# Optimization experiments

Hardware: AMD Instinct MI355X
Metric: run time of the kernel (lower is better)

## Reference

```python
import jax, jax.numpy as jnp
import numpy as np

NEG = -1e9


def _lstm_step(x, h, c, W_ih, W_hh, b_ih, b_hh):
    # torch LSTM gate order: i, f, g, o
    gates = x @ W_ih.T + b_ih + h @ W_hh.T + b_hh
    i, f, g, o = jnp.split(gates, 4, axis=-1)
    c_new = jax.nn.sigmoid(f) * c + jax.nn.sigmoid(i) * jnp.tanh(g)
    h_new = jax.nn.sigmoid(o) * jnp.tanh(c_new)
    return h_new, c_new


def _forward(encoder_states, emb, W_ih, W_hh, b_ih, b_hh, W_att,
             pad_mask, pointer_mask, token_ids, target_sequence,
             sos_token, eos_token, output_len):
    B, N, D = encoder_states.shape
    V = emb.shape[0]
    dt = encoder_states.dtype
    padf = pad_mask.astype(dt)
    enc = encoder_states * padf[..., None]          # zero padded node states
    # _init_lstm_state: mean of encoder states over valid nodes (pad-only mask)
    h0 = enc.sum(axis=1) / padf.sum(axis=1, keepdims=True)  # [B, D]
    # attention mask after pointer restriction: only valid leaf pointer nodes
    attn_mask = jnp.where(pointer_mask, jnp.asarray(0.0, dt), jnp.asarray(NEG, dt))
    n_ptr = pointer_mask.sum(axis=1).astype(dt)     # [B]
    thr = 1.0 / n_ptr                               # _threshold_cf = 1.0
    b_idx = jnp.arange(B)

    # teacher forcing: step 1 uses SOS, step s>1 uses target_sequence[s-1]
    sos_row = jnp.full((1, B), sos_token, dtype=target_sequence.dtype)
    inputs = jnp.concatenate([sos_row, target_sequence[1:output_len - 1]], axis=0)  # [T-1, B]

    def step(carry, inp):
        h, c = carry
        x = emb[inp]                                     # [B, E]
        h, c = _lstm_step(x, h, c, W_ih, W_hh, b_ih, b_hh)
        # Luong attention -> probabilities over tree nodes
        scores = jnp.einsum('bnd,bd->bn', enc, h @ W_att.T) + attn_mask
        probs = jax.nn.softmax(scores, axis=1)           # [B, N]
        # threshold: probabilities below 1/n_ptr are zeroed; only pointer nodes kept
        probs = jnp.where(pointer_mask & (probs >= thr[:, None]), probs, jnp.asarray(0.0, dt))
        # scatter(reduce='sum') node probabilities into vocab-sized output
        out = jnp.zeros((B, V), dt).at[b_idx[:, None], token_ids].add(probs)
        out = out.at[:, eos_token].set(1.0 - probs.sum(axis=1))
        return (h, c), out

    (_, _), outs = jax.lax.scan(step, (h0, h0), inputs)   # [T-1, B, V]
    out0 = jnp.zeros((B, V), dt).at[:, sos_token].set(1.0)
    return jnp.concatenate([out0[None], outs], axis=0)    # [T, B, V]


def setup_inputs() -> dict:
    key = jax.random.key(0)
    ks = jax.random.split(key, 10)
    B, N, D, E, V, T = 32, 2048, 512, 512, 32000, 32
    encoder_states = jax.random.normal(ks[0], (B, N, D), dtype=jnp.float32)
    lengths = jax.random.randint(ks[1], (B,), N // 2, N + 1)
    pad_mask = jnp.arange(N)[None, :] < lengths[:, None]            # [B, N] ragged trees
    leaf = jax.random.bernoulli(ks[2], 0.5, (B, N))
    pointer_mask = pad_mask & leaf                                  # valid leaf pointer nodes
    token_ids = jax.random.randint(ks[3], (B, N), 0, V, dtype=jnp.int32)
    target_sequence = jax.random.randint(ks[4], (T, B), 3, V, dtype=jnp.int32)
    s = 0.02
    emb = jax.random.normal(ks[5], (V, E), dtype=jnp.float32) * s
    W_ih = jax.random.normal(ks[6], (4 * D, E), dtype=jnp.float32) * s
    W_hh = jax.random.normal(ks[7], (4 * D, D), dtype=jnp.float32) * s
    b_ih = jnp.zeros((4 * D,), dtype=jnp.float32)
    b_hh = jnp.zeros((4 * D,), dtype=jnp.float32)
    W_att = jax.random.normal(ks[8], (D, D), dtype=jnp.float32) * s
    return {
        'encoder_states': encoder_states, 'emb': emb,
        'W_ih': W_ih, 'W_hh': W_hh, 'b_ih': b_ih, 'b_hh': b_hh, 'W_att': W_att,
        'pad_mask': pad_mask, 'pointer_mask': pointer_mask,
        'token_ids': token_ids, 'target_sequence': target_sequence,
        'sos_token': 1, 'eos_token': 2, 'output_len': T,
    }


def reference(encoder_states, emb, W_ih, W_hh, b_ih, b_hh, W_att,
              pad_mask, pointer_mask, token_ids, target_sequence,
              sos_token, eos_token, output_len):
    return _forward(encoder_states, emb, W_ih, W_hh, b_ih, b_hh, W_att,
                    pad_mask, pointer_mask, token_ids, target_sequence,
                    sos_token, eos_token, output_len)
```

## Files before the change

### kernel.cpp

```cpp
#include <hip/hip_runtime.h>
#include <math.h>

#define BB 32
#define NN 2048
#define DD 512
#define VV 32000
#define NSTEP 31

__device__ inline float sigm(float x){ return 1.0f/(1.0f+expf(-x)); }
__device__ inline float dot4(float4 a, float4 b){
  return a.x*b.x + a.y*b.y + a.z*b.z + a.w*b.w;
}

__device__ inline float red8(float a0,float a1,float a2,float a3,
                             float a4,float a5,float a6,float a7,int lane){
  float m01 = ((lane&1)? a1:a0) + __shfl_xor(((lane&1)? a0:a1),1,64);
  float m23 = ((lane&1)? a3:a2) + __shfl_xor(((lane&1)? a2:a3),1,64);
  float m45 = ((lane&1)? a5:a4) + __shfl_xor(((lane&1)? a4:a5),1,64);
  float m67 = ((lane&1)? a7:a6) + __shfl_xor(((lane&1)? a6:a7),1,64);
  float m03 = ((lane&2)? m23:m01) + __shfl_xor(((lane&2)? m01:m23),2,64);
  float m47 = ((lane&2)? m67:m45) + __shfl_xor(((lane&2)? m45:m67),2,64);
  float m   = ((lane&4)? m47:m03) + __shfl_xor(((lane&4)? m03:m47),4,64);
  m += __shfl_xor(m,8,64); m += __shfl_xor(m,16,64); m += __shfl_xor(m,32,64);
  return m;
}

__global__ __launch_bounds__(256) void k_cnt(
    const int* __restrict__ pad, const int* __restrict__ pmask,
    const int* __restrict__ sosp,
    float* __restrict__ cntp, float* __restrict__ thr, float* __restrict__ out,
    unsigned int* __restrict__ flags) {
  __shared__ int r1[256], r2[256];
  int b = blockIdx.x, tid = threadIdx.x;
  if (b == 0 && tid <= 256)
    __hip_atomic_store(&flags[tid], 0u, __ATOMIC_RELAXED,
                       __HIP_MEMORY_SCOPE_AGENT);
  float4* orow4 = (float4*)(out + (size_t)b*VV);
  float4 z = {0.f,0.f,0.f,0.f};
  for (int i = tid; i < VV/4; i += 256) orow4[i] = z;
  int cp = 0, cq = 0;
  for (int n = tid; n < NN; n += 256) { cp += pad[b*NN+n]; cq += pmask[b*NN+n]; }
  r1[tid] = cp; r2[tid] = cq; __syncthreads();
  for (int st = 128; st; st >>= 1) {
    if (tid < st) { r1[tid] += r1[tid+st]; r2[tid] += r2[tid+st]; }
    __syncthreads();
  }
  if (tid == 0) {
    cntp[b] = (float)r1[0];
    thr[b]  = 1.0f/(float)r2[0];
    out[(size_t)b*VV + sosp[0]] = 1.0f;
  }
}

__global__ __launch_bounds__(128) void k_meanpart(
    const float* __restrict__ enc, const int* __restrict__ pad,
    float* __restrict__ hpart) {
  int b = blockIdx.x, ch = blockIdx.y, kq = threadIdx.x;
  int n0 = ch*32;
  float4 acc = {0.f,0.f,0.f,0.f};
#pragma unroll 8
  for (int r = 0; r < 32; r++) {
    int n = n0 + r;
    float msk = (float)pad[b*NN + n];
    float4 v = *(const float4*)(enc + ((size_t)(b*NN + n))*DD + kq*4);
    acc.x += msk*v.x; acc.y += msk*v.y; acc.z += msk*v.z; acc.w += msk*v.w;
  }
  *(float4*)(hpart + ((size_t)(b*64 + ch))*DD + kq*4) = acc;
}

__global__ __launch_bounds__(128) void k_meanfin(
    const float* __restrict__ hpart, const float* __restrict__ cntp,
    float* __restrict__ h0, float* __restrict__ c) {
  int b = blockIdx.x, kq = threadIdx.x;
  float4 acc = {0.f,0.f,0.f,0.f};
  for (int ch = 0; ch < 64; ch++) {
    float4 v = *(const float4*)(hpart + ((size_t)(b*64 + ch))*DD + kq*4);
    acc.x += v.x; acc.y += v.y; acc.z += v.z; acc.w += v.w;
  }
  float ic = 1.0f/cntp[b];
  acc.x *= ic; acc.y *= ic; acc.z *= ic; acc.w *= ic;
  *(float4*)(h0 + b*DD + kq*4) = acc;
  *(float4*)(c  + b*DD + kq*4) = acc;
}

__global__ __launch_bounds__(256) void k_g0(
    const float* __restrict__ emb, const float* __restrict__ Wih,
    const float* __restrict__ bih, const float* __restrict__ bhh,
    const int* __restrict__ target, const int* __restrict__ sosp,
    float* __restrict__ G0) {
  int nt = blockIdx.x, mg = blockIdx.y;
  int w = threadIdx.x>>6, lane = threadIdx.x&63;
  int m0 = mg*32 + w*8;
  float4 x0[8], x1[8];
#pragma unroll
  for (int j = 0; j < 8; j++) {
    int m = m0 + j, s = m >> 5, bb = m & 31;
    int tok = (s == 0) ? sosp[0] : target[s*BB + bb];
    const float* xp = emb + (size_t)tok*DD + lane*4;
    x0[j] = *(const float4*)xp;
    x1[j] = *(const float4*)(xp + 256);
  }
  int r0 = nt*32;
#pragma unroll 2
  for (int i = 0; i < 32; i++) {
    int r = r0 + i;
    const float* wp = Wih + (size_t)r*DD + lane*4;
    float4 w0 = *(const float4*)wp, w1 = *(const float4*)(wp + 256);
    float a0 = dot4(w0,x0[0]) + dot4(w1,x1[0]);
    float a1 = dot4(w0,x0[1]) + dot4(w1,x1[1]);
    float a2 = dot4(w0,x0[2]) + dot4(w1,x1[2]);
    float a3 = dot4(w0,x0[3]) + dot4(w1,x1[3]);
    float a4 = dot4(w0,x0[4]) + dot4(w1,x1[4]);
    float a5 = dot4(w0,x0[5]) + dot4(w1,x1[5]);
    float a6 = dot4(w0,x0[6]) + dot4(w1,x1[6]);
    float a7 = dot4(w0,x0[7]) + dot4(w1,x1[7]);
    float v = red8(a0,a1,a2,a3,a4,a5,a6,a7,lane) + bih[r] + bhh[r];
    if (lane < 8) G0[(size_t)(m0 + lane)*2048 + r] = v;
  }
}

__global__ __launch_bounds__(512, 2) void k_hloop(
    const float* __restrict__ h0, const float* __restrict__ Whh,
    const float* __restrict__ G0, float* __restrict__ H,
    unsigned int* __restrict__ flags) {
  __shared__ float pad[20736];
  float* g = pad;
  int bi = blockIdx.x, d0 = bi*2;
  int tid = threadIdx.x;
  int w = tid>>6, lane = tid&63;
  float4 W0[8], W1[8];
#pragma unroll
  for (int j = 0; j < 8; j++) {
    int r = (j>>1)*DD + d0 + (j&1);
    const float* wp = Whh + (size_t)r*DD + lane*4;
    W0[j] = *(const float4*)wp; W1[j] = *(const float4*)(wp + 256);
  }
  int pb = tid>>1, pdd = tid&1;
  float creg = 0.f;
  if (tid < 64) creg = h0[pb*DD + d0 + pdd];

  for (int s = 0; s < NSTEP; s++) {
#pragma unroll
    for (int j = 0; j < 8; j++) {
      asm volatile("" : "+v"(W0[j].x), "+v"(W0[j].y),
                        "+v"(W0[j].z), "+v"(W0[j].w),
                        "+v"(W1[j].x), "+v"(W1[j].y),
                        "+v"(W1[j].z), "+v"(W1[j].w));
    }
    const float* hin = (s == 0) ? h0 : (H + (size_t)(s-1)*BB*DD);
    float Gi = 0.f, Gf = 0.f, Gg = 0.f, Go = 0.f;
    if (tid < 64) {
      const float* G = G0 + ((size_t)s*BB + pb)*2048 + d0 + pdd;
      Gi = G[0]; Gf = G[512]; Gg = G[1024]; Go = G[1536];
    }
#pragma unroll
    for (int bb = 0; bb < 4; bb++) {
      int b = w*4 + bb;
      const float* hp = hin + b*DD + lane*4;
      float4 h0v = *(const float4*)hp, h1v = *(const float4*)(hp + 256);
      float a0 = dot4(h0v,W0[0]) + dot4(h1v,W1[0]);
      float a1 = dot4(h0v,W0[1]) + dot4(h1v,W1[1]);
      float a2 = dot4(h0v,W0[2]) + dot4(h1v,W1[2]);
      float a3 = dot4(h0v,W0[3]) + dot4(h1v,W1[3]);
      float a4 = dot4(h0v,W0[4]) + dot4(h1v,W1[4]);
      float a5 = dot4(h0v,W0[5]) + dot4(h1v,W1[5]);
      float a6 = dot4(h0v,W0[6]) + dot4(h1v,W1[6]);
      float a7 = dot4(h0v,W0[7]) + dot4(h1v,W1[7]);
      float v = red8(a0,a1,a2,a3,a4,a5,a6,a7,lane);
      if (lane < 8) g[b*8 + lane] = v;
    }
    __syncthreads();
    if (tid < 64) {
      float gi = g[pb*8 + 0 + pdd] + Gi;
      float gf = g[pb*8 + 2 + pdd] + Gf;
      float gg = g[pb*8 + 4 + pdd] + Gg;
      float go = g[pb*8 + 6 + pdd] + Go;
      creg = sigm(gf)*creg + sigm(gi)*tanhf(gg);
      float hn = sigm(go)*tanhf(creg);
      __hip_atomic_store(H + (size_t)s*BB*DD + pb*DD + d0 + pdd, hn,
                         __ATOMIC_RELAXED, __HIP_MEMORY_SCOPE_AGENT);
    }
    if (s == NSTEP-1) break;
    __syncthreads();
    unsigned tgt = (unsigned)(s+1);
    if (tid == 0)
      __hip_atomic_store(&flags[bi], tgt,
                         __ATOMIC_RELAXED, __HIP_MEMORY_SCOPE_AGENT);
    if (bi == 0 && tid < 64) {
      const unsigned int* fp = flags + tid*4;
      for (;;) {
        unsigned f0 = __hip_atomic_load(fp+0, __ATOMIC_RELAXED,
                                        __HIP_MEMORY_SCOPE_AGENT);
        unsigned f1 = __hip_atomic_load(fp+1, __ATOMIC_RELAXED,
                                        __HIP_MEMORY_SCOPE_AGENT);
        unsigned f2 = __hip_atomic_load(fp+2, __ATOMIC_RELAXED,
                                        __HIP_MEMORY_SCOPE_AGENT);
        unsigned f3 = __hip_atomic_load(fp+3, __ATOMIC_RELAXED,
                                        __HIP_MEMORY_SCOPE_AGENT);
        if (f0 >= tgt && f1 >= tgt && f2 >= tgt && f3 >= tgt) break;
        __builtin_amdgcn_s_sleep(1);
      }
      if (tid == 0)
        __hip_atomic_store(&flags[256], tgt,
                           __ATOMIC_RELAXED, __HIP_MEMORY_SCOPE_AGENT);
    }
    if (tid == 0) {
      while (__hip_atomic_load(&flags[256], __ATOMIC_RELAXED,
                               __HIP_MEMORY_SCOPE_AGENT) < tgt)
        __builtin_amdgcn_s_sleep(1);
    }
    __syncthreads();
    if (tid == 0) {
      unsigned acq = __hip_atomic_load(&flags[256], __ATOMIC_ACQUIRE,
                                       __HIP_MEMORY_SCOPE_AGENT);
      asm volatile("" :: "v"(acq));
    }
    __syncthreads();
  }
}

__global__ __launch_bounds__(256) void k_qallw(
    const float* __restrict__ H, const float* __restrict__ Watt,
    float* __restrict__ Q) {
  int nt = blockIdx.x, mg = blockIdx.y;
  int w = threadIdx.x>>6, lane = threadIdx.x&63;
  int m0 = mg*32 + w*8;
  float4 x0[8], x1[8];
#pragma unroll
  for (int j = 0; j < 8; j++) {
    const float* xp = H + (size_t)(m0 + j)*DD + lane*4;
    x0[j] = *(const float4*)xp; x1[j] = *(const float4*)(xp + 256);
  }
  int r0 = nt*16;
#pragma unroll 2
  for (int i = 0; i < 16; i++) {
    int r = r0 + i;
    const float* wp = Watt + (size_t)r*DD + lane*4;
    float4 w0 = *(const float4*)wp, w1 = *(const float4*)(wp + 256);
    float a0 = dot4(w0,x0[0]) + dot4(w1,x1[0]);
    float a1 = dot4(w0,x0[1]) + dot4(w1,x1[1]);
    float a2 = dot4(w0,x0[2]) + dot4(w1,x1[2]);
    float a3 = dot4(w0,x0[3]) + dot4(w1,x1[3]);
    float a4 = dot4(w0,x0[4]) + dot4(w1,x1[4]);
    float a5 = dot4(w0,x0[5]) + dot4(w1,x1[5]);
    float a6 = dot4(w0,x0[6]) + dot4(w1,x1[6]);
    float a7 = dot4(w0,x0[7]) + dot4(w1,x1[7]);
    float v = red8(a0,a1,a2,a3,a4,a5,a6,a7,lane);
    if (lane < 8) Q[(size_t)(m0 + lane)*DD + r] = v;
  }
}

__global__ __launch_bounds__(256) void k_scores3(
    const float* __restrict__ enc, const float* __restrict__ Q,
    float* __restrict__ S) {
  int nt = blockIdx.x, b = blockIdx.y;
  int w = threadIdx.x>>6, lane = threadIdx.x&63;
  int s0 = w*8;
  float4 q0[8], q1[8];
#pragma unroll
  for (int j = 0; j < 8; j++) {
    const float* qp = Q + (size_t)((s0 + j)*BB + b)*DD + lane*4;
    q0[j] = *(const float4*)qp; q1[j] = *(const float4*)(qp + 256);
  }
  int n0 = nt*32;
  int sl = s0 + (lane & 7);
#pragma unroll 2
  for (int i = 0; i < 32; i++) {
    int n = n0 + i;
    const float* ep = enc + ((size_t)(b*NN + n))*DD + lane*4;
    float4 e0 = *(const float4*)ep, e1 = *(const float4*)(ep + 256);
    float a0 = dot4(e0,q0[0]) + dot4(e1,q1[0]);
    float a1 = dot4(e0,q0[1]) + dot4(e1,q1[1]);
    float a2 = dot4(e0,q0[2]) + dot4(e1,q1[2]);
    float a3 = dot4(e0,q0[3]) + dot4(e1,q1[3]);
    float a4 = dot4(e0,q0[4]) + dot4(e1,q1[4]);
    float a5 = dot4(e0,q0[5]) + dot4(e1,q1[5]);
    float a6 = dot4(e0,q0[6]) + dot4(e1,q1[6]);
    float a7 = dot4(e0,q0[7]) + dot4(e1,q1[7]);
    float v = red8(a0,a1,a2,a3,a4,a5,a6,a7,lane);
    if (lane < 8 && sl < NSTEP) S[((size_t)sl*BB + b)*NN + n] = v;
  }
}

__global__ __launch_bounds__(256) void k_scatter2(
    const float* __restrict__ S, const int* __restrict__ pmask,
    const int* __restrict__ tok, const float* __restrict__ thr,
    const int* __restrict__ eosp, float* __restrict__ out) {
  __shared__ float red[256];
  __shared__ float ex[NN];
  int s = blockIdx.x, b = blockIdx.y, tid = threadIdx.x;
  float* orow = out + ((size_t)(s+1)*BB + b)*VV;
  float4 z = {0.f,0.f,0.f,0.f};
  float4* orow4 = (float4*)orow;
  for (int i = tid; i < VV/4; i += 256) orow4[i] = z;
  const float* sr = S + ((size_t)s*BB + b)*NN;
  const int* pm = pmask + b*NN;
  float m = -3.4e38f;
  for (int n = tid; n < NN; n += 256) if (pm[n]) m = fmaxf(m, sr[n]);
  red[tid] = m; __syncthreads();
  for (int st = 128; st; st >>= 1) {
    if (tid < st) red[tid] = fmaxf(red[tid], red[tid+st]);
    __syncthreads();
  }
  float smax = red[0]; __syncthreads();
  float sum = 0.f;
  for (int n = tid; n < NN; n += 256) {
    float e = pm[n] ? expf(sr[n] - smax) : 0.f;
    ex[n] = e; sum += e;
  }
  red[tid] = sum; __syncthreads();
  for (int st = 128; st; st >>= 1) {
    if (tid < st) red[tid] += red[tid+st];
    __syncthreads();
  }
  float inv = 1.0f/red[0];
  float th = thr[b];
  float keep = 0.f;
  for (int n = tid; n < NN; n += 256) {
    float p = ex[n]*inv;
    if (p >= th) { atomicAdd(orow + tok[b*NN + n], p); keep += p; }
  }
  __syncthreads();
  red[tid] = keep; __syncthreads();
  for (int st = 128; st; st >>= 1) {
    if (tid < st) red[tid] += red[tid+st];
    __syncthreads();
  }
  if (tid == 0) orow[eosp[0]] = 1.0f - red[0];
}

extern "C" void kernel_launch(void* const* d_in, const int* in_sizes, int n_in,
                              void* d_out, int out_size, void* d_ws, size_t ws_size,
                              hipStream_t stream) {
  const float* enc   = (const float*)d_in[0];
  const float* emb   = (const float*)d_in[1];
  const float* Wih   = (const float*)d_in[2];
  const float* Whh   = (const float*)d_in[3];
  const float* bih   = (const float*)d_in[4];
  const float* bhh   = (const float*)d_in[5];
  const float* Watt  = (const float*)d_in[6];
  const int*   pad   = (const int*)d_in[7];
  const int*   pmask = (const int*)d_in[8];
  const int*   tok   = (const int*)d_in[9];
  const int*   target= (const int*)d_in[10];
  const int*   sosp  = (const int*)d_in[11];
  const int*   eosp  = (const int*)d_in[12];
  float* out = (float*)d_out;

  float* w    = (float*)d_ws;
  float* c    = w;
  float* h0   = c    + BB*DD;
  float* H    = h0   + BB*DD;
  float* Q    = H    + NSTEP*BB*DD;
  float* S    = Q    + 32*BB*DD;
  float* G0   = S    + (size_t)NSTEP*BB*NN;
  float* cntp = G0   + (size_t)992*2048;
  float* thr  = cntp + 32;
  unsigned int* flags = (unsigned int*)(thr + 32);
  float* hpart = G0;

  k_cnt<<<32, 256, 0, stream>>>(pad, pmask, sosp, cntp, thr, out, flags);
  k_meanpart<<<dim3(32,64), 128, 0, stream>>>(enc, pad, hpart);
  k_meanfin<<<32, 128, 0, stream>>>(hpart, cntp, h0, c);

  k_g0<<<dim3(64,31), 256, 0, stream>>>(emb, Wih, bih, bhh, target, sosp, G0);

  k_hloop<<<256, 512, 0, stream>>>(h0, Whh, G0, H, flags);

  k_qallw<<<dim3(32,31), 256, 0, stream>>>(H, Watt, Q);
  k_scores3<<<dim3(64,32), 256, 0, stream>>>(enc, Q, S);
  k_scatter2<<<dim3(NSTEP,32), 256, 0, stream>>>(S, pmask, tok, thr, eosp, out);
}
```

Before: 667.0 us.

## Fuse input-gate projection into persistent LSTM loop and overlap with grid barrier

Removes the separate k_g0 kernel that precomputed x@W_ih for all steps. Each persistent k_hloop block now keeps its W_ih slice in registers and computes the next step's input gates while waiting at the grid barrier, double-buffering them in shared memory. It also drops one barrier/acquire stage in the step sync and fixes the flag-reset range. The cost is doubled register pressure, which may cause spills, and relaxed-only ordering on the H reads after the barrier.

```diff
diff --git a/kernel.cpp b/kernel.cpp
--- a/kernel.cpp
+++ b/kernel.cpp
@@ -32,9 +32,14 @@
     unsigned int* __restrict__ flags) {
   __shared__ int r1[256], r2[256];
   int b = blockIdx.x, tid = threadIdx.x;
-  if (b == 0 && tid <= 256)
-    __hip_atomic_store(&flags[tid], 0u, __ATOMIC_RELAXED,
-                       __HIP_MEMORY_SCOPE_AGENT);
+  if (b == 0) {
+    if (tid < 256)
+      __hip_atomic_store(&flags[tid], 0u, __ATOMIC_RELAXED,
+                         __HIP_MEMORY_SCOPE_AGENT);
+    if (tid == 0)
+      __hip_atomic_store(&flags[256], 0u, __ATOMIC_RELAXED,
+                         __HIP_MEMORY_SCOPE_AGENT);
+  }
   float4* orow4 = (float4*)(out + (size_t)b*VV);
   float4 z = {0.f,0.f,0.f,0.f};
   for (int i = tid; i < VV/4; i += 256) orow4[i] = z;
@@ -83,61 +88,54 @@
   *(float4*)(c  + b*DD + kq*4) = acc;
 }
 
-__global__ __launch_bounds__(256) void k_g0(
-    const float* __restrict__ emb, const float* __restrict__ Wih,
-    const float* __restrict__ bih, const float* __restrict__ bhh,
-    const int* __restrict__ target, const int* __restrict__ sosp,
-    float* __restrict__ G0) {
-  int nt = blockIdx.x, mg = blockIdx.y;
-  int w = threadIdx.x>>6, lane = threadIdx.x&63;
-  int m0 = mg*32 + w*8;
-  float4 x0[8], x1[8];
-#pragma unroll
-  for (int j = 0; j < 8; j++) {
-    int m = m0 + j, s = m >> 5, bb = m & 31;
-    int tok = (s == 0) ? sosp[0] : target[s*BB + bb];
-    const float* xp = emb + (size_t)tok*DD + lane*4;
-    x0[j] = *(const float4*)xp;
-    x1[j] = *(const float4*)(xp + 256);
-  }
-  int r0 = nt*32;
-#pragma unroll 2
-  for (int i = 0; i < 32; i++) {
-    int r = r0 + i;
-    const float* wp = Wih + (size_t)r*DD + lane*4;
-    float4 w0 = *(const float4*)wp, w1 = *(const float4*)(wp + 256);
-    float a0 = dot4(w0,x0[0]) + dot4(w1,x1[0]);
-    float a1 = dot4(w0,x0[1]) + dot4(w1,x1[1]);
-    float a2 = dot4(w0,x0[2]) + dot4(w1,x1[2]);
-    float a3 = dot4(w0,x0[3]) + dot4(w1,x1[3]);
-    float a4 = dot4(w0,x0[4]) + dot4(w1,x1[4]);
-    float a5 = dot4(w0,x0[5]) + dot4(w1,x1[5]);
-    float a6 = dot4(w0,x0[6]) + dot4(w1,x1[6]);
-    float a7 = dot4(w0,x0[7]) + dot4(w1,x1[7]);
-    float v = red8(a0,a1,a2,a3,a4,a5,a6,a7,lane) + bih[r] + bhh[r];
-    if (lane < 8) G0[(size_t)(m0 + lane)*2048 + r] = v;
-  }
-}
-
 __global__ __launch_bounds__(512, 2) void k_hloop(
     const float* __restrict__ h0, const float* __restrict__ Whh,
-    const float* __restrict__ G0, float* __restrict__ H,
-    unsigned int* __restrict__ flags) {
-  __shared__ float pad[20736];
-  float* g = pad;
+    const float* __restrict__ Wih, const float* __restrict__ bih,
+    const float* __restrict__ bhh, const float* __restrict__ emb,
+    const int* __restrict__ target, const int* __restrict__ sosp,
+    float* __restrict__ H, unsigned int* __restrict__ flags) {
+  __shared__ float spad[20736];
+  float* g   = spad;
+  float* Gls = spad + 256;
   int bi = blockIdx.x, d0 = bi*2;
   int tid = threadIdx.x;
   int w = tid>>6, lane = tid&63;
-  float4 W0[8], W1[8];
+  float4 W0[8], W1[8], Wi0[8], Wi1[8];
 #pragma unroll
   for (int j = 0; j < 8; j++) {
     int r = (j>>1)*DD + d0 + (j&1);
     const float* wp = Whh + (size_t)r*DD + lane*4;
-    W0[j] = *(const float4*)wp; W1[j] = *(const float4*)(wp + 256);
-  }
+    W0[j]  = *(const float4*)wp; W1[j]  = *(const float4*)(wp + 256);
+    const float* ip = Wih + (size_t)r*DD + lane*4;
+    Wi0[j] = *(const float4*)ip; Wi1[j] = *(const float4*)(ip + 256);
+  }
+  int jrole = lane & 7;
+  int brow = (jrole>>1)*DD + d0 + (jrole&1);
+  float biasj = bih[brow] + bhh[brow];
   int pb = tid>>1, pdd = tid&1;
   float creg = 0.f;
   if (tid < 64) creg = h0[pb*DD + d0 + pdd];
+
+  {
+    int sos = sosp[0];
+    const float* xp = emb + (size_t)sos*DD + lane*4;
+    float4 x0 = *(const float4*)xp, x1 = *(const float4*)(xp + 256);
+    float a0 = dot4(x0,Wi0[0]) + dot4(x1,Wi1[0]);
+    float a1 = dot4(x0,Wi0[1]) + dot4(x1,Wi1[1]);
+    float a2 = dot4(x0,Wi0[2]) + dot4(x1,Wi1[2]);
+    float a3 = dot4(x0,Wi0[3]) + dot4(x1,Wi1[3]);
+    float a4 = dot4(x0,Wi0[4]) + dot4(x1,Wi1[4]);
+    float a5 = dot4(x0,Wi0[5]) + dot4(x1,Wi1[5]);
+    float a6 = dot4(x0,Wi0[6]) + dot4(x1,Wi1[6]);
+    float a7 = dot4(x0,Wi0[7]) + dot4(x1,Wi1[7]);
+    float v = red8(a0,a1,a2,a3,a4,a5,a6,a7,lane);
+    if (lane < 8) {
+      float vb = v + biasj;
+#pragma unroll
+      for (int bb = 0; bb < 4; bb++) Gls[(w*4+bb)*8 + lane] = vb;
+    }
+  }
+  __syncthreads();
 
   for (int s = 0; s < NSTEP; s++) {
 #pragma unroll
@@ -146,13 +144,12 @@
                         "+v"(W0[j].z), "+v"(W0[j].w),
                         "+v"(W1[j].x), "+v"(W1[j].y),
                         "+v"(W1[j].z), "+v"(W1[j].w));
+      asm volatile("" : "+v"(Wi0[j].x), "+v"(Wi0[j].y),
+                        "+v"(Wi0[j].z), "+v"(Wi0[j].w),
+                        "+v"(Wi1[j].x), "+v"(Wi1[j].y),
+                        "+v"(Wi1[j].z), "+v"(Wi1[j].w));
     }
     const float* hin = (s == 0) ? h0 : (H + (size_t)(s-1)*BB*DD);
-    float Gi = 0.f, Gf = 0.f, Gg = 0.f, Go = 0.f;
-    if (tid < 64) {
-      const float* G = G0 + ((size_t)s*BB + pb)*2048 + d0 + pdd;
-      Gi = G[0]; Gf = G[512]; Gg = G[1024]; Go = G[1536];
-    }
 #pragma unroll
     for (int bb = 0; bb < 4; bb++) {
       int b = w*4 + bb;
@@ -169,12 +166,22 @@
       float v = red8(a0,a1,a2,a3,a4,a5,a6,a7,lane);
       if (lane < 8) g[b*8 + lane] = v;
     }
+    float4 xg0[4], xg1[4];
+    if (s < NSTEP-1) {
+#pragma unroll
+      for (int bb = 0; bb < 4; bb++) {
+        int tg = target[(s+1)*BB + w*4 + bb];
+        const float* xp = emb + (size_t)tg*DD + lane*4;
+        xg0[bb] = *(const float4*)xp; xg1[bb] = *(const float4*)(xp + 256);
+      }
+    }
     __syncthreads();
     if (tid < 64) {
-      float gi = g[pb*8 + 0 + pdd] + Gi;
-      float gf = g[pb*8 + 2 + pdd] + Gf;
-      float gg = g[pb*8 + 4 + pdd] + Gg;
-      float go = g[pb*8 + 6 + pdd] + Go;
+      const float* Gs = Gls + (s&1)*256;
+      float gi = g[pb*8 + 0 + pdd] + Gs[pb*8 + 0 + pdd];
+      float gf = g[pb*8 + 2 + pdd] + Gs[pb*8 + 2 + pdd];
+      float gg = g[pb*8 + 4 + pdd] + Gs[pb*8 + 4 + pdd];
+      float go = g[pb*8 + 6 + pdd] + Gs[pb*8 + 6 + pdd];
       creg = sigm(gf)*creg + sigm(gi)*tanhf(gg);
       float hn = sigm(go)*tanhf(creg);
       __hip_atomic_store(H + (size_t)s*BB*DD + pb*DD + d0 + pdd, hn,
@@ -186,6 +193,22 @@
     if (tid == 0)
       __hip_atomic_store(&flags[bi], tgt,
                          __ATOMIC_RELAXED, __HIP_MEMORY_SCOPE_AGENT);
+    {
+      float* Gd = Gls + ((s+1)&1)*256;
+#pragma unroll
+      for (int bb = 0; bb < 4; bb++) {
+        float a0 = dot4(xg0[bb],Wi0[0]) + dot4(xg1[bb],Wi1[0]);
+        float a1 = dot4(xg0[bb],Wi0[1]) + dot4(xg1[bb],Wi1[1]);
+        float a2 = dot4(xg0[bb],Wi0[2]) + dot4(xg1[bb],Wi1[2]);
+        float a3 = dot4(xg0[bb],Wi0[3]) + dot4(xg1[bb],Wi1[3]);
+        float a4 = dot4(xg0[bb],Wi0[4]) + dot4(xg1[bb],Wi1[4]);
+        float a5 = dot4(xg0[bb],Wi0[5]) + dot4(xg1[bb],Wi1[5]);
+        float a6 = dot4(xg0[bb],Wi0[6]) + dot4(xg1[bb],Wi1[6]);
+        float a7 = dot4(xg0[bb],Wi0[7]) + dot4(xg1[bb],Wi1[7]);
+        float v = red8(a0,a1,a2,a3,a4,a5,a6,a7,lane);
+        if (lane < 8) Gd[(w*4+bb)*8 + lane] = v + biasj;
+      }
+    }
     if (bi == 0 && tid < 64) {
       const unsigned int* fp = flags + tid*4;
       for (;;) {
@@ -208,12 +231,6 @@
       while (__hip_atomic_load(&flags[256], __ATOMIC_RELAXED,
                                __HIP_MEMORY_SCOPE_AGENT) < tgt)
         __builtin_amdgcn_s_sleep(1);
-    }
-    __syncthreads();
-    if (tid == 0) {
-      unsigned acq = __hip_atomic_load(&flags[256], __ATOMIC_ACQUIRE,
-                                       __HIP_MEMORY_SCOPE_AGENT);
-      asm volatile("" :: "v"(acq));
     }
     __syncthreads();
   }
@@ -363,9 +380,8 @@
   k_meanpart<<<dim3(32,64), 128, 0, stream>>>(enc, pad, hpart);
   k_meanfin<<<32, 128, 0, stream>>>(hpart, cntp, h0, c);
 
-  k_g0<<<dim3(64,31), 256, 0, stream>>>(emb, Wih, bih, bhh, target, sosp, G0);
-
-  k_hloop<<<256, 512, 0, stream>>>(h0, Whh, G0, H, flags);
+  k_hloop<<<256, 512, 0, stream>>>(h0, Whh, Wih, bih, bhh, emb, target, sosp,
+                                   H, flags);
 
   k_qallw<<<dim3(32,31), 256, 0, stream>>>(H, Watt, Q);
   k_scores3<<<dim3(64,32), 256, 0, stream>>>(enc, Q, S);
```

Result: faster. 602.5 us (-9.7%).
